# Performance work log

Hardware: AMD Instinct MI355X
Metric: run time of the kernel (lower is better)

The kernel has to match this reference:

```python
import jax, jax.numpy as jnp
import numpy as np
from jax import lax

EPS = 1e-5  # BatchNorm / LayerNorm eps
B, DIM, H, W = 32, 256, 64, 64
S = 64            # state_dim
D_INNER = 256     # ssd_expand * dim
HIDDEN = 1024     # mlp_ratio * dim


def _bn(x, g, b, m, v):
    # BatchNorm2d, inference mode with given running stats. x: (B,C,H,W)
    inv = lax.rsqrt(v + EPS)
    return (x - m[None, :, None, None]) * (g * inv)[None, :, None, None] + b[None, :, None, None]


def _dwconv3x3(x, w):
    # depthwise 3x3 conv, stride 1, SAME padding. w: (C,1,3,3)
    return lax.conv_general_dilated(
        x, w, window_strides=(1, 1), padding='SAME',
        feature_group_count=x.shape[1],
        dimension_numbers=('NCHW', 'OIHW', 'NCHW'))


def setup_inputs() -> dict:
    key = jax.random.key(0)
    ks = jax.random.split(key, 32)
    n = lambda i, shp, s=0.02: jax.random.normal(ks[i], shp, jnp.float32) * s
    u = lambda i, shp: jax.random.uniform(ks[i], shp, jnp.float32)
    return {
        'x': jax.random.normal(ks[0], (B, DIM, H, W), jnp.float32),
        # dwconv1 (Conv2dNorm depthwise)
        'dw1_w': n(1, (DIM, 1, 3, 3)), 'dw1_g': 1.0 + n(2, (DIM,)), 'dw1_b': n(3, (DIM,)),
        'dw1_m': n(4, (DIM,)), 'dw1_v': u(5, (DIM,)) + 0.5,
        # LayerNorm1d
        'ln_w': 1.0 + n(6, (DIM,)), 'ln_b': n(7, (DIM,)),
        # mixer (HSMSSD)
        'bcdt_w': n(8, (3 * S, DIM)),
        'dwm_w': n(9, (3 * S, 1, 3, 3)),
        'A_param': 1.0 + 15.0 * u(10, (S,)),
        'hz_w': n(11, (2 * D_INNER, DIM)),
        'out_w': n(12, (DIM, D_INNER)),
        'D_param': jnp.ones((1,), jnp.float32),
        # dwconv2
        'dw2_w': n(13, (DIM, 1, 3, 3)), 'dw2_g': 1.0 + n(14, (DIM,)), 'dw2_b': n(15, (DIM,)),
        'dw2_m': n(16, (DIM,)), 'dw2_v': u(17, (DIM,)) + 0.5,
        # FFN
        'fc1_w': n(18, (HIDDEN, DIM)), 'fc1_g': 1.0 + n(19, (HIDDEN,)), 'fc1_b': n(20, (HIDDEN,)),
        'fc1_m': n(21, (HIDDEN,)), 'fc1_v': u(22, (HIDDEN,)) + 0.5,
        'fc2_w': n(23, (DIM, HIDDEN)), 'fc2_g': 1.0 + n(24, (DIM,)), 'fc2_b': n(25, (DIM,)),
        'fc2_m': n(26, (DIM,)), 'fc2_v': u(27, (DIM,)) + 0.5,
        # alpha-gated residual blends
        'alpha': 1e-4 * jnp.ones((4, DIM), jnp.float32) + n(28, (4, DIM), 0.01),
    }


def reference(x, dw1_w, dw1_g, dw1_b, dw1_m, dw1_v, ln_w, ln_b,
              bcdt_w, dwm_w, A_param, hz_w, out_w, D_param,
              dw2_w, dw2_g, dw2_b, dw2_m, dw2_v,
              fc1_w, fc1_g, fc1_b, fc1_m, fc1_v,
              fc2_w, fc2_g, fc2_b, fc2_m, fc2_v, alpha):
    b, dim, h_, w_ = x.shape
    L = h_ * w_
    a = jax.nn.sigmoid(alpha)[:, :, None, None]  # (4, dim, 1, 1)

    # alpha-blended depthwise conv 1
    x = (1.0 - a[0]) * x + a[0] * _bn(_dwconv3x3(x, dw1_w), dw1_g, dw1_b, dw1_m, dw1_v)
    x_prev = x

    # LayerNorm1d over channel dim on (B, C, L)
    xf = x.reshape(b, dim, L)
    mean = xf.mean(axis=1, keepdims=True)
    var = ((xf - mean) ** 2).mean(axis=1, keepdims=True)
    xn = (xf - mean) * lax.rsqrt(var + EPS) * ln_w[None, :, None] + ln_b[None, :, None]

    # HSMSSD mixer
    bc_dt = jnp.einsum('bcl,oc->bol', xn, bcdt_w).reshape(b, 3 * S, h_, w_)
    bc_dt = _dwconv3x3(bc_dt, dwm_w).reshape(b, 3 * S, L)
    Bm, Cm, dt = jnp.split(bc_dt, 3, axis=1)          # each (B, S, L)
    Am = jax.nn.softmax(dt + A_param[None, :, None], axis=-1)
    AB = Am * Bm                                      # (B, S, L)
    h = jnp.einsum('bcl,bsl->bcs', xn, AB)            # (B, dim, S)
    hz = jnp.einsum('bcs,oc->bos', h, hz_w)           # (B, 2*d_inner, S)
    hh, z = jnp.split(hz, 2, axis=1)
    hg = hh * jax.nn.silu(z) + hh * D_param[0]
    hout = jnp.einsum('bcs,oc->bos', hg, out_w)       # (B, dim, S)
    y = jnp.einsum('bcs,bsl->bcl', hout, Cm).reshape(b, dim, h_, w_)

    x = (1.0 - a[1]) * x_prev + a[1] * y
    x = (1.0 - a[2]) * x + a[2] * _bn(_dwconv3x3(x, dw2_w), dw2_g, dw2_b, dw2_m, dw2_v)

    # FFN: 1x1 conv + BN + ReLU + 1x1 conv + BN
    t = _bn(jnp.einsum('bchw,oc->bohw', x, fc1_w), fc1_g, fc1_b, fc1_m, fc1_v)
    t = jax.nn.relu(t)
    t = _bn(jnp.einsum('bchw,oc->bohw', t, fc2_w), fc2_g, fc2_b, fc2_m, fc2_v)
    x = (1.0 - a[3]) * x + a[3] * t
    return (x, hout)
```

## Files before the change

### kernel.cpp

```cpp
#include <hip/hip_runtime.h>
#include <hip/hip_bf16.h>

typedef __hip_bfloat16 bf16;
typedef __attribute__((ext_vector_type(8))) short bf16x8;
typedef __attribute__((ext_vector_type(4))) float f32x4;

__device__ __forceinline__ float LD(const float* p){ return *p; }
__device__ __forceinline__ float LD(const bf16* p){ return __bfloat162float(*p); }
__device__ __forceinline__ void ST(float* p, float v){ *p = v; }
__device__ __forceinline__ void ST(bf16* p, float v){ *p = __float2bfloat16(v); }
__device__ __forceinline__ float sigm(float v){ return 1.f/(1.f + expf(-v)); }
__device__ __forceinline__ ushort f2b(float f){
    unsigned u = __float_as_uint(f);
    return (ushort)((u + 0x7fffu + ((u>>16)&1u)) >> 16);
}

#define NEPS 1e-5f

__global__ __launch_bounds__(256) void dwconv_bn_blend(
        const float* __restrict__ xin, float* __restrict__ xout,
        const float* __restrict__ w, const float* __restrict__ gg, const float* __restrict__ bb,
        const float* __restrict__ mm, const float* __restrict__ vv,
        const float* __restrict__ alpha, int arow)
{
    __shared__ float tile[66*66];
    int blk = blockIdx.x;
    int ch = blk & 255;
    const float* xp = xin + (size_t)blk*4096;
    float* op = xout + (size_t)blk*4096;
    int tid = threadIdx.x;
    for (int i = tid; i < 66*66; i += 256) {
        int r = i/66, c = i%66;
        int gr = r-1, gc = c-1;
        float val = 0.f;
        if (gr >= 0 && gr < 64 && gc >= 0 && gc < 64) val = xp[gr*64+gc];
        tile[i] = val;
    }
    __syncthreads();
    float wv[9];
    #pragma unroll
    for (int k=0;k<9;k++) wv[k] = w[ch*9+k];
    float sc = gg[ch] * rsqrtf(vv[ch] + NEPS);
    float mv = mm[ch], bv = bb[ch];
    float av = sigm(alpha[arow*256+ch]);
    for (int p = tid; p < 4096; p += 256) {
        int r = p>>6, c = p&63;
        float a = 0.f;
        #pragma unroll
        for (int dr=0;dr<3;dr++)
            #pragma unroll
            for (int dc=0;dc<3;dc++)
                a += wv[dr*3+dc]*tile[(r+dr)*66 + (c+dc)];
        float bn = (a - mv)*sc + bv;
        float xv = tile[(r+1)*66 + (c+1)];
        op[p] = (1.f-av)*xv + av*bn;
    }
}

__global__ __launch_bounds__(256) void ln_stats(const float* __restrict__ x1,
        float* __restrict__ meanp, float* __restrict__ invp)
{
    int blk = blockIdx.x;
    int b = blk >> 4;
    int l = ((blk & 15) << 8) + threadIdx.x;
    const float* xp = x1 + (size_t)b*256*4096 + l;
    float mean = 0.f, m2 = 0.f;
    for (int c=0;c<256;c++){ float v = xp[(size_t)c*4096]; mean += v; m2 += v*v; }
    mean *= (1.f/256.f); m2 *= (1.f/256.f);
    meanp[b*4096 + l] = mean;
    invp[b*4096 + l] = rsqrtf(m2 - mean*mean + NEPS);
}

__global__ __launch_bounds__(256) void prep_k(
        const float* __restrict__ f1w, const float* __restrict__ f2w,
        const float* __restrict__ bcdtw,
        const float* __restrict__ g1, const float* __restrict__ b1,
        const float* __restrict__ m1, const float* __restrict__ v1,
        const float* __restrict__ g2, const float* __restrict__ b2,
        const float* __restrict__ m2, const float* __restrict__ v2,
        ushort* __restrict__ w1bf, ushort* __restrict__ w2bf,
        ushort* __restrict__ wbc,
        float* __restrict__ sc1, float* __restrict__ sb1,
        float* __restrict__ sc2, float* __restrict__ sb2)
{
    int i = blockIdx.x*256 + threadIdx.x;
    if (i < 262144) {
        w1bf[i] = f2b(f1w[i]);
        w2bf[i] = f2b(f2w[i]);
    }
    if (i < 49152) wbc[i] = f2b(bcdtw[i]);
    if (i < 1024) { float s = g1[i]*rsqrtf(v1[i]+NEPS); sc1[i]=s; sb1[i]=b1[i]-m1[i]*s; }
    if (i < 256)  { float s = g2[i]*rsqrtf(v2[i]+NEPS); sc2[i]=s; sb2[i]=b2[i]-m2[i]*s; }
}

__global__ __launch_bounds__(256) void bcdt_mfma(
        const float* __restrict__ x1,
        const float* __restrict__ meanp, const float* __restrict__ invp,
        const float* __restrict__ lnw, const float* __restrict__ lnb,
        const ushort* __restrict__ wbc,
        bf16* __restrict__ bc, ushort* __restrict__ xn_bf, int b0)
{
    __shared__ __align__(16) ushort Xs[64*256];
    int blk = blockIdx.x;
    int lb = blk >> 6;
    int b  = b0 + lb;
    int l0 = (blk & 63) << 6;
    int tid = threadIdx.x, lane = tid & 63, w = tid >> 6;
    const float* xp = x1 + (size_t)b*256*4096 + l0;
    float mval = meanp[b*4096 + l0 + lane];
    float ival = invp [b*4096 + l0 + lane];
    ushort* xnp = xn_bf + (size_t)lb*256*4096 + l0;

    for (int cc = w*8; cc < 256; cc += 32) {
        ushort u[8];
        #pragma unroll
        for (int j=0;j<8;j++){
            float v = xp[(size_t)(cc+j)*4096 + lane];
            float xn = (v - mval)*ival*lnw[cc+j] + lnb[cc+j];
            u[j] = f2b(xn);
            xnp[(size_t)(cc+j)*4096 + lane] = u[j];
        }
        uint4 pk;
        pk.x = (uint)u[0] | ((uint)u[1]<<16);
        pk.y = (uint)u[2] | ((uint)u[3]<<16);
        pk.z = (uint)u[4] | ((uint)u[5]<<16);
        pk.w = (uint)u[6] | ((uint)u[7]<<16);
        int g = (cc>>3) ^ (lane&7);
        *(uint4*)&Xs[lane*256 + g*8] = pk;
    }
    __syncthreads();

    f32x4 zero4 = {0.f,0.f,0.f,0.f};
    f32x4 acc[3][4];
    #pragma unroll
    for (int m=0;m<3;m++)
        #pragma unroll
        for (int f=0;f<4;f++) acc[m][f] = zero4;

    int hbase = w*48;
    for (int ks=0; ks<8; ks++){
        bf16x8 afr[3];
        #pragma unroll
        for (int m=0;m<3;m++)
            afr[m] = *(const bf16x8*)&wbc[(size_t)(hbase + m*16 + (lane&15))*256
                                          + ks*32 + (lane>>4)*8];
        #pragma unroll
        for (int f=0;f<4;f++){
            int px = f*16 + (lane&15);
            int g = (ks*4 + (lane>>4)) ^ (px&7);
            bf16x8 bfr = *(const bf16x8*)&Xs[px*256 + g*8];
            #pragma unroll
            for (int m=0;m<3;m++)
                acc[m][f] = __builtin_amdgcn_mfma_f32_16x16x32_bf16(afr[m], bfr, acc[m][f], 0,0,0);
        }
    }
    bf16* op = bc + (size_t)lb*192*4096 + l0;
    #pragma unroll
    for (int m=0;m<3;m++)
        #pragma unroll
        for (int r=0;r<4;r++){
            int o = hbase + m*16 + (lane>>4)*4 + r;
            #pragma unroll
            for (int f=0;f<4;f++){
                int px = f*16 + (lane&15);
                op[(size_t)o*4096 + px] = __float2bfloat16(acc[m][f][r]);
            }
        }
}

__global__ __launch_bounds__(256) void dwconv_plain(bf16* __restrict__ data, const float* __restrict__ w)
{
    __shared__ float tile[66*66];
    int blk = blockIdx.x;
    int ch = blk % 192;
    bf16* xp = data + (size_t)blk*4096;
    int tid = threadIdx.x;
    for (int i = tid; i < 66*66; i += 256) {
        int r = i/66, c = i%66;
        int gr = r-1, gc = c-1;
        float val = 0.f;
        if (gr >= 0 && gr < 64 && gc >= 0 && gc < 64) val = LD(&xp[gr*64+gc]);
        tile[i] = val;
    }
    __syncthreads();
    float wv[9];
    #pragma unroll
    for (int k=0;k<9;k++) wv[k] = w[ch*9+k];
    for (int p = tid; p < 4096; p += 256) {
        int r = p>>6, c = p&63;
        float a = 0.f;
        #pragma unroll
        for (int dr=0;dr<3;dr++)
            #pragma unroll
            for (int dc=0;dc<3;dc++)
                a += wv[dr*3+dc]*tile[(r+dr)*66 + (c+dc)];
        ST(&xp[p], a);
    }
}

__global__ __launch_bounds__(256) void softmax_ab(bf16* __restrict__ bc, const float* __restrict__ A)
{
    __shared__ float red[8];
    int blk = blockIdx.x;
    int lb = blk >> 6;
    int s = blk & 63;
    bf16* dtp = bc + ((size_t)lb*192 + 128 + s)*4096;
    bf16* bmp = bc + ((size_t)lb*192 + s)*4096;
    int tid = threadIdx.x;
    float Av = A[s];
    float vals[16];
    float mx = -1e30f;
    #pragma unroll
    for (int i=0;i<16;i++){ vals[i] = LD(&dtp[i*256+tid]) + Av; mx = fmaxf(mx, vals[i]); }
    #pragma unroll
    for (int o=32;o>0;o>>=1) mx = fmaxf(mx, __shfl_down(mx, o));
    int lane = tid & 63, wid = tid >> 6;
    if (lane == 0) red[wid] = mx;
    __syncthreads();
    if (tid == 0) red[4] = fmaxf(fmaxf(red[0],red[1]), fmaxf(red[2],red[3]));
    __syncthreads();
    mx = red[4];
    float sum = 0.f;
    #pragma unroll
    for (int i=0;i<16;i++){ vals[i] = expf(vals[i]-mx); sum += vals[i]; }
    #pragma unroll
    for (int o=32;o>0;o>>=1) sum += __shfl_down(sum, o);
    if (lane == 0) red[wid] = sum;
    __syncthreads();
    if (tid == 0) red[5] = red[0]+red[1]+red[2]+red[3];
    __syncthreads();
    float inv = 1.f/red[5];
    #pragma unroll
    for (int i=0;i<16;i++){
        float ab = vals[i]*inv*LD(&bmp[i*256+tid]);
        ST(&bmp[i*256+tid], ab);
    }
}

__global__ __launch_bounds__(256) void h_mfma(
        const ushort* __restrict__ xn_bf, const bf16* __restrict__ bc,
        float* __restrict__ h_part)
{
    int blk = blockIdx.x;
    int lb = blk >> 3;
    int kz = blk & 7;
    int kbase = kz*512;
    int tid = threadIdx.x, lane = tid & 63, w = tid >> 6;
    const ushort* ap = xn_bf + (size_t)lb*256*4096;
    const ushort* bp = (const ushort*)bc + (size_t)lb*192*4096;
    f32x4 zero4 = {0.f,0.f,0.f,0.f};
    f32x4 acc[4][4];
    #pragma unroll
    for (int m=0;m<4;m++)
        #pragma unroll
        for (int n=0;n<4;n++) acc[m][n] = zero4;

    for (int ks=0; ks<16; ks++){
        int koff = kbase + ks*32 + (lane>>4)*8;
        bf16x8 afr[4], bfr[4];
        #pragma unroll
        for (int m=0;m<4;m++)
            afr[m] = *(const bf16x8*)&ap[(size_t)(w*64 + m*16 + (lane&15))*4096 + koff];
        #pragma unroll
        for (int n=0;n<4;n++)
            bfr[n] = *(const bf16x8*)&bp[(size_t)(n*16 + (lane&15))*4096 + koff];
        #pragma unroll
        for (int m=0;m<4;m++)
            #pragma unroll
            for (int n=0;n<4;n++)
                acc[m][n] = __builtin_amdgcn_mfma_f32_16x16x32_bf16(afr[m], bfr[n], acc[m][n], 0,0,0);
    }
    float* hp = h_part + ((size_t)lb*8 + kz)*16384;
    #pragma unroll
    for (int m=0;m<4;m++)
        #pragma unroll
        for (int n=0;n<4;n++)
            #pragma unroll
            for (int r=0;r<4;r++){
                int c = w*64 + m*16 + (lane>>4)*4 + r;
                int s = n*16 + (lane&15);
                hp[c*64 + s] = acc[m][n][r];
            }
}

__global__ __launch_bounds__(256) void hz_gemm(const float* __restrict__ h_part,
        const float* __restrict__ w, float* __restrict__ hz)
{
    __shared__ float ht[256][64];
    int blk = blockIdx.x; int lb = blk>>3; int o0 = (blk&7)*64;
    int tid = threadIdx.x;
    const float* hp = h_part + (size_t)lb*8*16384;
    for (int i=tid;i<16384;i+=256){
        float s = 0.f;
        #pragma unroll
        for (int k=0;k<8;k++) s += hp[k*16384 + i];
        ht[i>>6][i&63] = s;
    }
    __syncthreads();
    int lane=tid&63, g=tid>>6;
    for (int i4=0;i4<4;i4++){
        int ol = g*16 + i4*4;
        const float* r0 = w + (size_t)(o0+ol)*256;
        const float *r1=r0+256, *r2=r0+512, *r3=r0+768;
        float d0=0.f,d1=0.f,d2=0.f,d3=0.f;
        #pragma unroll 8
        for (int c4=0;c4<64;c4++){
            float x0=ht[c4*4][lane],x1v=ht[c4*4+1][lane],x2v=ht[c4*4+2][lane],x3v=ht[c4*4+3][lane];
            float4 a0=((const float4*)r0)[c4],a1=((const float4*)r1)[c4];
            float4 a2=((const float4*)r2)[c4],a3=((const float4*)r3)[c4];
            d0 += a0.x*x0+a0.y*x1v+a0.z*x2v+a0.w*x3v;
            d1 += a1.x*x0+a1.y*x1v+a1.z*x2v+a1.w*x3v;
            d2 += a2.x*x0+a2.y*x1v+a2.z*x2v+a2.w*x3v;
            d3 += a3.x*x0+a3.y*x1v+a3.z*x2v+a3.w*x3v;
        }
        size_t base = ((size_t)lb*512 + o0 + ol)*64 + lane;
        hz[base]=d0; hz[base+64]=d1; hz[base+128]=d2; hz[base+192]=d3;
    }
}

__global__ void gate_k(const float* __restrict__ hz, float* __restrict__ hg, const float* __restrict__ Dp)
{
    int i = blockIdx.x*256 + threadIdx.x;
    int lb = i >> 14;
    int r = i & 16383;
    const float* hp = hz + (size_t)lb*32768;
    float hh = hp[r], z = hp[16384 + r];
    float sil = z / (1.f + expf(-z));
    hg[i] = hh * (sil + Dp[0]);
}

__global__ __launch_bounds__(256) void out_gemm(const float* __restrict__ hg, const float* __restrict__ w,
        ushort* __restrict__ hout_bf, float* __restrict__ hout_out, int b0)
{
    __shared__ float ht[256][64];
    int blk = blockIdx.x; int lb = blk>>2; int b = b0 + lb; int o0 = (blk&3)*64;
    int tid = threadIdx.x;
    const float* hp = hg + (size_t)lb*16384;
    for (int i=tid;i<16384;i+=256) ht[i>>6][i&63]=hp[i];
    __syncthreads();
    int lane=tid&63, g=tid>>6;
    for (int i4=0;i4<4;i4++){
        int ol = g*16 + i4*4;
        const float* r0 = w + (size_t)(o0+ol)*256;
        const float *r1=r0+256, *r2=r0+512, *r3=r0+768;
        float d0=0.f,d1=0.f,d2=0.f,d3=0.f;
        #pragma unroll 8
        for (int c4=0;c4<64;c4++){
            float x0=ht[c4*4][lane],x1v=ht[c4*4+1][lane],x2v=ht[c4*4+2][lane],x3v=ht[c4*4+3][lane];
            float4 a0=((const float4*)r0)[c4],a1=((const float4*)r1)[c4];
            float4 a2=((const float4*)r2)[c4],a3=((const float4*)r3)[c4];
            d0 += a0.x*x0+a0.y*x1v+a0.z*x2v+a0.w*x3v;
            d1 += a1.x*x0+a1.y*x1v+a1.z*x2v+a1.w*x3v;
            d2 += a2.x*x0+a2.y*x1v+a2.z*x2v+a2.w*x3v;
            d3 += a3.x*x0+a3.y*x1v+a3.z*x2v+a3.w*x3v;
        }
        size_t lbase = ((size_t)lb*256 + o0 + ol)*64 + lane;
        hout_bf[lbase]=f2b(d0); hout_bf[lbase+64]=f2b(d1);
        hout_bf[lbase+128]=f2b(d2); hout_bf[lbase+192]=f2b(d3);
        size_t gbase = ((size_t)b*256 + o0 + ol)*64 + lane;
        hout_out[gbase]=d0; hout_out[gbase+64]=d1;
        hout_out[gbase+128]=d2; hout_out[gbase+192]=d3;
    }
}

__global__ __launch_bounds__(256) void y_mfma(
        const ushort* __restrict__ hout_bf, const bf16* __restrict__ bc,
        float* __restrict__ x1, const float* __restrict__ alpha, int b0)
{
    __shared__ __align__(16) ushort Cs[64*64];
    int blk = blockIdx.x; int lb = blk>>6; int b = b0 + lb; int l0 = (blk&63)<<6;
    int tid = threadIdx.x, lane = tid&63, w = tid>>6;
    const ushort* cp = (const ushort*)bc + ((size_t)lb*192 + 64)*4096 + l0;
    for (int sc = w*8; sc < 64; sc += 32){
        ushort u[8];
        #pragma unroll
        for (int j=0;j<8;j++) u[j] = cp[(size_t)(sc+j)*4096 + lane];
        uint4 pk;
        pk.x = (uint)u[0] | ((uint)u[1]<<16);
        pk.y = (uint)u[2] | ((uint)u[3]<<16);
        pk.z = (uint)u[4] | ((uint)u[5]<<16);
        pk.w = (uint)u[6] | ((uint)u[7]<<16);
        int g = (sc>>3) ^ (lane&7);
        *(uint4*)&Cs[lane*64 + g*8] = pk;
    }
    __syncthreads();

    f32x4 zero4 = {0.f,0.f,0.f,0.f};
    f32x4 acc[4][4];
    #pragma unroll
    for (int m=0;m<4;m++)
        #pragma unroll
        for (int f=0;f<4;f++) acc[m][f] = zero4;

    const ushort* ap = hout_bf + (size_t)lb*256*64;
    #pragma unroll
    for (int ks=0; ks<2; ks++){
        bf16x8 afr[4];
        #pragma unroll
        for (int m=0;m<4;m++)
            afr[m] = *(const bf16x8*)&ap[(size_t)(w*64 + m*16 + (lane&15))*64
                                          + ks*32 + (lane>>4)*8];
        #pragma unroll
        for (int f=0;f<4;f++){
            int px = f*16 + (lane&15);
            int s8 = ks*32 + (lane>>4)*8;
            int g = (s8>>3) ^ (px&7);
            bf16x8 bfr = *(const bf16x8*)&Cs[px*64 + g*8];
            #pragma unroll
            for (int m=0;m<4;m++)
                acc[m][f] = __builtin_amdgcn_mfma_f32_16x16x32_bf16(afr[m], bfr, acc[m][f], 0,0,0);
        }
    }

    float* xpo = x1 + (size_t)b*256*4096 + l0;
    #pragma unroll
    for (int m=0;m<4;m++)
        #pragma unroll
        for (int r=0;r<4;r++){
            int c = w*64 + m*16 + (lane>>4)*4 + r;
            float av = sigm(alpha[256+c]);
            #pragma unroll
            for (int f=0;f<4;f++){
                int px = f*16 + (lane&15);
                float xv = xpo[(size_t)c*4096 + px];
                xpo[(size_t)c*4096 + px] = (1.f-av)*xv + av*acc[m][f][r];
            }
        }
}

__global__ __launch_bounds__(256) void ffn_mfma(
        const float* __restrict__ x,
        const ushort* __restrict__ w1bf,
        const ushort* __restrict__ w2bf,
        const float* __restrict__ sc1, const float* __restrict__ sb1,
        const float* __restrict__ sc2, const float* __restrict__ sb2,
        const float* __restrict__ alpha,
        float* __restrict__ out)
{
    __shared__ __align__(16) ushort Xs[64*256];
    __shared__ __align__(16) ushort Ts[64*128];
    int blk = blockIdx.x;
    int b = blk >> 6, l0 = (blk & 63) << 6;
    int tid = threadIdx.x, lane = tid & 63, w = tid >> 6;
    const float* xp = x + (size_t)b*256*4096 + l0;

    for (int cc = w*8; cc < 256; cc += 32) {
        float v[8];
        #pragma unroll
        for (int j=0;j<8;j++) v[j] = xp[(size_t)(cc+j)*4096 + lane];
        uint4 pk;
        pk.x = (uint)f2b(v[0]) | ((uint)f2b(v[1])<<16);
        pk.y = (uint)f2b(v[2]) | ((uint)f2b(v[3])<<16);
        pk.z = (uint)f2b(v[4]) | ((uint)f2b(v[5])<<16);
        pk.w = (uint)f2b(v[6]) | ((uint)f2b(v[7])<<16);
        int g = (cc>>3) ^ (lane&7);
        *(uint4*)&Xs[lane*256 + g*8] = pk;
    }
    __syncthreads();

    f32x4 zero4 = {0.f,0.f,0.f,0.f};
    f32x4 acc2[4][4];
    #pragma unroll
    for (int m=0;m<4;m++)
        #pragma unroll
        for (int f=0;f<4;f++) acc2[m][f] = zero4;

    for (int hc = 0; hc < 1024; hc += 128) {
        int hbase = hc + w*32;
        f32x4 c1[2][4];
        #pragma unroll
        for (int m=0;m<2;m++)
            #pragma unroll
            for (int f=0;f<4;f++) c1[m][f] = zero4;
        for (int ks = 0; ks < 8; ks++) {
            bf16x8 afr[2];
            #pragma unroll
            for (int m=0;m<2;m++)
                afr[m] = *(const bf16x8*)&w1bf[(size_t)(hbase + m*16 + (lane&15))*256
                                               + ks*32 + (lane>>4)*8];
            #pragma unroll
            for (int f=0;f<4;f++){
                int px = f*16 + (lane&15);
                int g = (ks*4 + (lane>>4)) ^ (px&7);
                bf16x8 bfr = *(const bf16x8*)&Xs[px*256 + g*8];
                #pragma unroll
                for (int m=0;m<2;m++)
                    c1[m][f] = __builtin_amdgcn_mfma_f32_16x16x32_bf16(afr[m], bfr, c1[m][f], 0,0,0);
            }
        }
        __syncthreads();
        #pragma unroll
        for (int m=0;m<2;m++){
            #pragma unroll
            for (int r=0;r<4;r++){
                int h = hbase + m*16 + (lane>>4)*4 + r;
                float s1 = sc1[h], bb1 = sb1[h];
                int hl = h - hc;
                #pragma unroll
                for (int f=0;f<4;f++){
                    int px = f*16 + (lane&15);
                    float t = fmaxf(c1[m][f][r]*s1 + bb1, 0.f);
                    int g = (hl>>3) ^ (px&7);
                    Ts[px*128 + g*8 + (hl&7)] = f2b(t);
                }
            }
        }
        __syncthreads();
        int c0 = w*64;
        for (int ks = 0; ks < 4; ks++) {
            bf16x8 afr[4];
            #pragma unroll
            for (int m=0;m<4;m++)
                afr[m] = *(const bf16x8*)&w2bf[(size_t)(c0 + m*16 + (lane&15))*1024
                                               + hc + ks*32 + (lane>>4)*8];
            #pragma unroll
            for (int f=0;f<4;f++){
                int px = f*16 + (lane&15);
                int hl = ks*32 + (lane>>4)*8;
                int g = (hl>>3) ^ (px&7);
                bf16x8 bfr = *(const bf16x8*)&Ts[px*128 + g*8];
                #pragma unroll
                for (int m=0;m<4;m++)
                    acc2[m][f] = __builtin_amdgcn_mfma_f32_16x16x32_bf16(afr[m], bfr, acc2[m][f], 0,0,0);
            }
        }
    }

    float* op = out + (size_t)b*256*4096 + l0;
    int c0 = w*64;
    #pragma unroll
    for (int m=0;m<4;m++){
        #pragma unroll
        for (int r=0;r<4;r++){
            int c = c0 + m*16 + (lane>>4)*4 + r;
            float a = sigm(alpha[768+c]);
            float s2 = sc2[c], bb2 = sb2[c];
            #pragma unroll
            for (int f=0;f<4;f++){
                int px = f*16 + (lane&15);
                float t2 = acc2[m][f][r]*s2 + bb2;
                float xv = xp[(size_t)c*4096 + px];
                op[(size_t)c*4096 + px] = (1.f-a)*xv + a*t2;
            }
        }
    }
}

extern "C" void kernel_launch(void* const* d_in, const int* in_sizes, int n_in,
                              void* d_out, int out_size, void* d_ws, size_t ws_size,
                              hipStream_t stream)
{
    (void)in_sizes; (void)n_in; (void)out_size;
    const float* x     = (const float*)d_in[0];
    const float* dw1w  = (const float*)d_in[1];
    const float* dw1g  = (const float*)d_in[2];
    const float* dw1b  = (const float*)d_in[3];
    const float* dw1m  = (const float*)d_in[4];
    const float* dw1v  = (const float*)d_in[5];
    const float* lnw   = (const float*)d_in[6];
    const float* lnb   = (const float*)d_in[7];
    const float* bcdtw = (const float*)d_in[8];
    const float* dwmw  = (const float*)d_in[9];
    const float* Ap    = (const float*)d_in[10];
    const float* hzw   = (const float*)d_in[11];
    const float* outw  = (const float*)d_in[12];
    const float* Dp    = (const float*)d_in[13];
    const float* dw2w  = (const float*)d_in[14];
    const float* dw2g  = (const float*)d_in[15];
    const float* dw2b  = (const float*)d_in[16];
    const float* dw2m  = (const float*)d_in[17];
    const float* dw2v  = (const float*)d_in[18];
    const float* f1w   = (const float*)d_in[19];
    const float* f1g   = (const float*)d_in[20];
    const float* f1b   = (const float*)d_in[21];
    const float* f1m   = (const float*)d_in[22];
    const float* f1v   = (const float*)d_in[23];
    const float* f2w   = (const float*)d_in[24];
    const float* f2g   = (const float*)d_in[25];
    const float* f2b_  = (const float*)d_in[26];
    const float* f2m   = (const float*)d_in[27];
    const float* f2v   = (const float*)d_in[28];
    const float* alpha = (const float*)d_in[29];

    const size_t nx = (size_t)32*256*4096;
    float* x1 = (float*)d_out;
    float* hout_out = x1 + nx;

    char* ws = (char*)d_ws;
    float* meanp = (float*)ws;
    float* invp  = meanp + 131072;
    size_t off = 1048576;
    ushort* w1bf = (ushort*)(ws + off); off += 524288;
    ushort* w2bf = (ushort*)(ws + off); off += 524288;
    ushort* wbc  = (ushort*)(ws + off); off += 98304;
    float* sc1 = (float*)(ws + off); off += 4096;
    float* sb1 = (float*)(ws + off); off += 4096;
    float* sc2 = (float*)(ws + off); off += 1024;
    float* sb2 = (float*)(ws + off); off += 1024;
    off = (off + 255) & ~(size_t)255;
    char* cbase = ws + off;
    size_t avail = ws_size > off ? ws_size - off : 0;

    const size_t perb = 1572864 + 2097152 + 524288 + 131072 + 65536 + 32768;
    int NB = 1;
    for (int nb = 32; nb >= 1; nb >>= 1) if (avail >= (size_t)nb*perb) { NB = nb; break; }

    prep_k<<<1024,256,0,stream>>>(f1w, f2w, bcdtw, f1g,f1b,f1m,f1v, f2g,f2b_,f2m,f2v,
                                  w1bf, w2bf, wbc, sc1, sb1, sc2, sb2);
    dwconv_bn_blend<<<8192,256,0,stream>>>(x, x1, dw1w,dw1g,dw1b,dw1m,dw1v, alpha, 0);
    ln_stats<<<512,256,0,stream>>>(x1, meanp, invp);

    bf16*   bc      = (bf16*)cbase;
    ushort* xn_bf   = (ushort*)(cbase + (size_t)NB*1572864);
    float*  h_part  = (float*)(cbase + (size_t)NB*(1572864 + 2097152));
    float*  hz      = (float*)((char*)h_part + (size_t)NB*524288);
    float*  hg      = (float*)((char*)hz + (size_t)NB*131072);
    ushort* hout_bf = (ushort*)((char*)hg + (size_t)NB*65536);

    for (int b0 = 0; b0 < 32; b0 += NB) {
        bcdt_mfma<<<NB*64,256,0,stream>>>(x1, meanp, invp, lnw, lnb, wbc, bc, xn_bf, b0);
        dwconv_plain<<<NB*192,256,0,stream>>>(bc, dwmw);
        softmax_ab<<<NB*64,256,0,stream>>>(bc, Ap);
        h_mfma<<<NB*8,256,0,stream>>>(xn_bf, bc, h_part);
        hz_gemm<<<NB*8,256,0,stream>>>(h_part, hzw, hz);
        gate_k<<<NB*64,256,0,stream>>>(hz, hg, Dp);
        out_gemm<<<NB*4,256,0,stream>>>(hg, outw, hout_bf, hout_out, b0);
        y_mfma<<<NB*64,256,0,stream>>>(hout_bf, bc, x1, alpha, b0);
    }

    dwconv_bn_blend<<<8192,256,0,stream>>>(x1, x1, dw2w,dw2g,dw2b,dw2m,dw2v, alpha, 2);
    ffn_mfma<<<2048,256,0,stream>>>(x1, w1bf, w2bf, sc1, sb1, sc2, sb2, alpha, x1);
}
```

Baseline: 734.6 us.

## Double-buffer FFN hidden tile to overlap GEMM1 and GEMM2 stages

Splits the FFN kernel into gemm1, writeTs and gemm2 stages and double-buffers the hidden-activation LDS tile. GEMM1 for the next chunk can then be interleaved with GEMM2 on the previous chunk, and each iteration needs one barrier instead of two. The BN+ReLU write-out also packs four bf16 values into one 8-byte LDS store instead of scalar stores. In exchange LDS use rises from 48KB to 64KB per block, which may lower occupancy.

```diff
diff --git a/kernel.cpp b/kernel.cpp
--- a/kernel.cpp
+++ b/kernel.cpp
@@ -438,7 +438,7 @@
         float* __restrict__ out)
 {
     __shared__ __align__(16) ushort Xs[64*256];
-    __shared__ __align__(16) ushort Ts[64*128];
+    __shared__ __align__(16) ushort Ts[2][64*128];
     int blk = blockIdx.x;
     int b = blk >> 6, l0 = (blk & 63) << 6;
     int tid = threadIdx.x, lane = tid & 63, w = tid >> 6;
@@ -464,14 +464,14 @@
     for (int m=0;m<4;m++)
         #pragma unroll
         for (int f=0;f<4;f++) acc2[m][f] = zero4;
-
-    for (int hc = 0; hc < 1024; hc += 128) {
+    f32x4 c1[2][4];
+
+    auto gemm1 = [&](int hc){
+        #pragma unroll
+        for (int m=0;m<2;m++)
+            #pragma unroll
+            for (int f=0;f<4;f++) c1[m][f] = zero4;
         int hbase = hc + w*32;
-        f32x4 c1[2][4];
-        #pragma unroll
-        for (int m=0;m<2;m++)
-            #pragma unroll
-            for (int f=0;f<4;f++) c1[m][f] = zero4;
         for (int ks = 0; ks < 8; ks++) {
             bf16x8 afr[2];
             #pragma unroll
@@ -488,24 +488,33 @@
                     c1[m][f] = __builtin_amdgcn_mfma_f32_16x16x32_bf16(afr[m], bfr, c1[m][f], 0,0,0);
             }
         }
-        __syncthreads();
+    };
+
+    auto writeTs = [&](int pp, int hc){
         #pragma unroll
         for (int m=0;m<2;m++){
-            #pragma unroll
-            for (int r=0;r<4;r++){
-                int h = hbase + m*16 + (lane>>4)*4 + r;
-                float s1 = sc1[h], bb1 = sb1[h];
-                int hl = h - hc;
-                #pragma unroll
-                for (int f=0;f<4;f++){
-                    int px = f*16 + (lane&15);
-                    float t = fmaxf(c1[m][f][r]*s1 + bb1, 0.f);
-                    int g = (hl>>3) ^ (px&7);
-                    Ts[px*128 + g*8 + (hl&7)] = f2b(t);
-                }
+            int hl0 = w*32 + m*16 + ((lane>>4)<<2);
+            int h0 = hc + hl0;
+            float s0=sc1[h0], s1=sc1[h0+1], s2=sc1[h0+2], s3=sc1[h0+3];
+            float q0=sb1[h0], q1=sb1[h0+1], q2=sb1[h0+2], q3=sb1[h0+3];
+            int gbase = hl0>>3;
+            #pragma unroll
+            for (int f=0;f<4;f++){
+                int px = f*16 + (lane&15);
+                float t0 = fmaxf(c1[m][f][0]*s0 + q0, 0.f);
+                float t1 = fmaxf(c1[m][f][1]*s1 + q1, 0.f);
+                float t2 = fmaxf(c1[m][f][2]*s2 + q2, 0.f);
+                float t3 = fmaxf(c1[m][f][3]*s3 + q3, 0.f);
+                uint2 pk;
+                pk.x = (uint)f2b(t0) | ((uint)f2b(t1)<<16);
+                pk.y = (uint)f2b(t2) | ((uint)f2b(t3)<<16);
+                int g = gbase ^ (px&7);
+                *(uint2*)&Ts[pp][px*128 + g*8 + (hl0&7)] = pk;
             }
         }
-        __syncthreads();
+    };
+
+    auto gemm2 = [&](int pp, int hc){
         int c0 = w*64;
         for (int ks = 0; ks < 4; ks++) {
             bf16x8 afr[4];
@@ -518,13 +527,26 @@
                 int px = f*16 + (lane&15);
                 int hl = ks*32 + (lane>>4)*8;
                 int g = (hl>>3) ^ (px&7);
-                bf16x8 bfr = *(const bf16x8*)&Ts[px*128 + g*8];
+                bf16x8 bfr = *(const bf16x8*)&Ts[pp][px*128 + g*8];
                 #pragma unroll
                 for (int m=0;m<4;m++)
                     acc2[m][f] = __builtin_amdgcn_mfma_f32_16x16x32_bf16(afr[m], bfr, acc2[m][f], 0,0,0);
             }
         }
-    }
+    };
+
+    gemm1(0);
+    writeTs(0, 0);
+    __syncthreads();
+    int p = 0;
+    for (int hc = 128; hc < 1024; hc += 128) {
+        gemm1(hc);
+        gemm2(p, hc-128);
+        writeTs(p^1, hc);
+        __syncthreads();
+        p ^= 1;
+    }
+    gemm2(p, 896);
 
     float* op = out + (size_t)b*256*4096 + l0;
     int c0 = w*64;
```

Result: slower. 803.6 us (+9.4%).
